# Optimization experiments

Hardware: AMD Instinct MI355X
Metric: run time of the kernel (lower is better)

The kernel has to match this reference:

```python
import jax, jax.numpy as jnp
import numpy as np

N = 50000
E = 1600000
IN = 128
HID = 128
OUT = 64
NL = 200000
NEG_SLOPE = 0.2


def _glorot(key, shape):
    fan_in, fan_out = shape[0], shape[-1]
    s = jnp.sqrt(6.0 / (fan_in + fan_out))
    return jax.random.uniform(key, shape, jnp.float32, -s, s)


def setup_inputs() -> dict:
    key = jax.random.key(0)
    ks = jax.random.split(key, 16)
    x = jax.random.normal(ks[0], (N, IN), jnp.float32)
    edge_index = jax.random.randint(ks[1], (2, E), 0, N, dtype=jnp.int32)
    edge_label_index = jax.random.randint(ks[2], (2, NL), 0, N, dtype=jnp.int32)
    return {
        "x": x,
        "edge_index": edge_index,
        "edge_label_index": edge_label_index,
        "W1": _glorot(ks[3], (IN, HID)),  "a1s": _glorot(ks[4], (HID,)),  "a1d": _glorot(ks[5], (HID,)),  "b1": jnp.zeros((HID,), jnp.float32),
        "W2": _glorot(ks[6], (HID, HID)), "a2s": _glorot(ks[7], (HID,)),  "a2d": _glorot(ks[8], (HID,)),  "b2": jnp.zeros((HID,), jnp.float32),
        "W3": _glorot(ks[9], (HID, HID)), "a3s": _glorot(ks[10], (HID,)), "a3d": _glorot(ks[11], (HID,)), "b3": jnp.zeros((HID,), jnp.float32),
        "W4": _glorot(ks[12], (HID, OUT)), "b4": jnp.zeros((OUT,), jnp.float32),
    }


def _add_self_loops(edge_index, n):
    loop = jnp.arange(n, dtype=edge_index.dtype)
    return jnp.concatenate([edge_index, jnp.stack([loop, loop])], axis=1)


def gat_conv(x, edge_index, W, a_s, a_d, b):
    """PyG GATConv, heads=1, add_self_loops=True: gather, LeakyReLU score,
    segment softmax over destination nodes, scatter-add aggregate."""
    n = x.shape[0]
    ei = _add_self_loops(edge_index, n)
    src, dst = ei[0], ei[1]
    h = x @ W                                    # [N, H]
    e = jax.nn.leaky_relu((h @ a_s)[src] + (h @ a_d)[dst], NEG_SLOPE)  # [E']
    m = jax.ops.segment_max(e, dst, num_segments=n)
    p = jnp.exp(e - m[dst])
    s = jax.ops.segment_sum(p, dst, num_segments=n)
    alpha = p / s[dst]                           # segment softmax
    out = jax.ops.segment_sum(h[src] * alpha[:, None], dst, num_segments=n)
    return out + b


def gcn_conv(x, edge_index, W, b):
    """PyG GCNConv: self-loops + symmetric degree normalization."""
    n = x.shape[0]
    ei = _add_self_loops(edge_index, n)
    src, dst = ei[0], ei[1]
    h = x @ W
    deg = jax.ops.segment_sum(jnp.ones(src.shape, h.dtype), dst, num_segments=n)
    dinv = jax.lax.rsqrt(deg)
    norm = dinv[src] * dinv[dst]                 # [E']
    out = jax.ops.segment_sum(h[src] * norm[:, None], dst, num_segments=n)
    return out + b


def reference(x, edge_index, edge_label_index,
              W1, a1s, a1d, b1, W2, a2s, a2d, b2,
              W3, a3s, a3d, b3, W4, b4):
    h = jax.nn.relu(gat_conv(x, edge_index, W1, a1s, a1d, b1))
    h = jax.nn.relu(gat_conv(h, edge_index, W2, a2s, a2d, b2))
    h = jax.nn.relu(gat_conv(h, edge_index, W3, a3s, a3d, b3))
    z = gcn_conv(h, edge_index, W4, b4)          # [N, OUT]
    # decode: dot product of endpoint embeddings -> link logits [NL]
    return (z[edge_label_index[0]] * z[edge_label_index[1]]).sum(axis=-1)
```

## Files before the change

### kernel.cpp

```cpp
#include <hip/hip_runtime.h>
#include <hip/hip_fp16.h>
#include <math.h>

#define NN   50000
#define NE   1600000
#define DHID 128
#define DOUTC 64
#define NLBL 200000
#define CAP  80
#define NEG  0.2f
#define NBK  196
#define CAPB 8800
#define CHK  4096

typedef unsigned short u16;
typedef _Float16 half8 __attribute__((ext_vector_type(8)));
typedef float floatx4 __attribute__((ext_vector_type(4)));


__global__ __launch_bounds__(256) void k_bin(const int* __restrict__ ei,
                                             int* __restrict__ gcnt,
                                             unsigned* __restrict__ bins) {
    __shared__ int cntL[NBK];
    __shared__ int curL[NBK];
    const int tid = threadIdx.x;
    const int e0 = blockIdx.x * CHK + tid * 16;
    const bool act = (e0 + 15) < NE;

    unsigned pk[16];
    int bb[16];
    if (act) {
#pragma unroll
        for (int g = 0; g < 4; ++g) {
            int4 s4 = *(const int4*)&ei[e0 + g * 4];
            int4 d4 = *(const int4*)&ei[NE + e0 + g * 4];
            int sa[4] = {s4.x, s4.y, s4.z, s4.w};
            int da[4] = {d4.x, d4.y, d4.z, d4.w};
#pragma unroll
            for (int k = 0; k < 4; ++k) {
                int idx = g * 4 + k;
                bb[idx] = da[k] >> 8;
                pk[idx] = (unsigned)sa[k] | ((unsigned)(da[k] & 255) << 16);
            }
        }
    }
    for (int i = tid; i < NBK; i += 256) cntL[i] = 0;
    __syncthreads();
    if (act) {
#pragma unroll
        for (int k = 0; k < 16; ++k) atomicAdd(&cntL[bb[k]], 1);
    }
    __syncthreads();
    for (int i = tid; i < NBK; i += 256) curL[i] = atomicAdd(&gcnt[i], cntL[i]);
    __syncthreads();
    if (act) {
#pragma unroll
        for (int k = 0; k < 16; ++k) {
            int off = atomicAdd(&curL[bb[k]], 1);
            bins[(size_t)bb[k] * CAPB + off] = pk[k];
        }
    }
}

__global__ __launch_bounds__(256) void k_build(const unsigned* __restrict__ bins,
                                               const int* __restrict__ gcnt,
                                               int* __restrict__ cnt,
                                               u16* __restrict__ csr) {
    __shared__ u16 rows[256 * CAP];
    __shared__ int cur[256];
    const int b = blockIdx.x, tid = threadIdx.x;
    const int d0 = b << 8;
    const int nd = min(256, NN - d0);
    if (tid < nd) { cur[tid] = 1; rows[tid * CAP] = (u16)(d0 + tid); }
    __syncthreads();
    const int n = gcnt[b];
    for (int i = tid; i < n; i += 256) {
        unsigned v = bins[(size_t)b * CAPB + i];
        int s = v & 0xFFFF, dl = v >> 16;
        int pos = atomicAdd(&cur[dl], 1);
        if (pos < CAP) rows[dl * CAP + pos] = (u16)s;
    }
    __syncthreads();
    const unsigned* rw = (const unsigned*)rows;
    unsigned* cw = (unsigned*)(csr + (size_t)d0 * CAP);
    const int tot = nd * (CAP / 2);
    for (int i = tid; i < tot; i += 256) cw[i] = rw[i];
    if (tid < nd) cnt[d0 + tid] = cur[tid];
}


__global__ __launch_bounds__(256) void k_prep_w(const float* __restrict__ W1f,
                                                const float* __restrict__ W2f,
                                                const float* __restrict__ W3f,
                                                const float* __restrict__ W4f,
                                                half8* __restrict__ Wf1,
                                                half8* __restrict__ Wf2,
                                                half8* __restrict__ Wf3,
                                                half8* __restrict__ Wf4,
                                                int* __restrict__ gcnt) {
    if (blockIdx.x == 28) {
        int i = threadIdx.x;
        if (i < NBK) gcnt[i] = 0;
        return;
    }
    int e = blockIdx.x * 256 + threadIdx.x;
    const float* W;
    half8* Wf;
    int nout, le;
    if (e < 2048)      { W = W1f; Wf = Wf1; nout = 128; le = e; }
    else if (e < 4096) { W = W2f; Wf = Wf2; nout = 128; le = e - 2048; }
    else if (e < 6144) { W = W3f; Wf = Wf3; nout = 128; le = e - 4096; }
    else               { W = W4f; Wf = Wf4; nout = 64;  le = e - 6144; }
    int c = le >> 8, rem = le & 255, ks = rem >> 6, lane = rem & 63;
    int n = lane & 15, quad = lane >> 4;
    int col = c * 16 + n, k0 = ks * 32 + quad * 8;
    half8 v;
#pragma unroll
    for (int j = 0; j < 8; ++j) v[j] = (_Float16)W[(size_t)(k0 + j) * nout + col];
    Wf[le] = v;
}


template <int NOUT, bool ATTN, typename TA>
__global__ __launch_bounds__(256) void gemm_mfma(const TA* __restrict__ Ain,
                                                 const half8* __restrict__ Wf,
                                                 __half* __restrict__ C16,
                                                 const float* __restrict__ a_s,
                                                 const float* __restrict__ a_d,
                                                 float* __restrict__ asv,
                                                 float* __restrict__ adv, int M) {
    constexpr int CT = NOUT / 16;
    const int tid = threadIdx.x;
    const int wave = tid >> 6, lane = tid & 63;
    const int n = lane & 15, quad = lane >> 4;
    const int row0 = blockIdx.x * 64 + wave * 16;

    const int row = row0 + n;
    const bool ok = row < M;
    half8 a[4];
    half8 zz = {};
#pragma unroll
    for (int ks = 0; ks < 4; ++ks) {
        if (!ok) { a[ks] = zz; continue; }
        if constexpr (sizeof(TA) == 2) {
            a[ks] = *(const half8*)((const _Float16*)Ain + (size_t)row * 128 + quad * 8 + ks * 32);
        } else {
            const float* Ap = (const float*)Ain + (size_t)row * 128 + quad * 8 + ks * 32;
            float4 f0 = *(const float4*)Ap;
            float4 f1 = *(const float4*)(Ap + 4);
            half8 v;
            v[0] = (_Float16)f0.x; v[1] = (_Float16)f0.y; v[2] = (_Float16)f0.z; v[3] = (_Float16)f0.w;
            v[4] = (_Float16)f1.x; v[5] = (_Float16)f1.y; v[6] = (_Float16)f1.z; v[7] = (_Float16)f1.w;
            a[ks] = v;
        }
    }

    floatx4 acc[CT];
#pragma unroll
    for (int c = 0; c < CT; ++c) acc[c] = (floatx4){0.f, 0.f, 0.f, 0.f};

#pragma unroll
    for (int c = 0; c < CT; ++c) {
#pragma unroll
        for (int ks = 0; ks < 4; ++ks) {
            half8 b = Wf[(c * 4 + ks) * 64 + lane];
            acc[c] = __builtin_amdgcn_mfma_f32_16x16x32_f16(b, a[ks], acc[c], 0, 0, 0);
        }
    }

    if (ok) {
#pragma unroll
        for (int c = 0; c < CT; ++c) {
            __half2 h0 = __floats2half2_rn(acc[c][0], acc[c][1]);
            __half2 h1 = __floats2half2_rn(acc[c][2], acc[c][3]);
            uint2 u;
            __builtin_memcpy(&u.x, &h0, 4);
            __builtin_memcpy(&u.y, &h1, 4);
            *(uint2*)&C16[(size_t)row * NOUT + c * 16 + quad * 4] = u;
        }
    }

    if (ATTN) {
        float ps = 0.f, pd = 0.f;
#pragma unroll
        for (int c = 0; c < CT; ++c) {
#pragma unroll
            for (int reg = 0; reg < 4; ++reg) {
                float w = acc[c][reg];
                ps = fmaf(w, a_s[c * 16 + quad * 4 + reg], ps);
                pd = fmaf(w, a_d[c * 16 + quad * 4 + reg], pd);
            }
        }
        ps += __shfl_xor(ps, 16); ps += __shfl_xor(ps, 32);
        pd += __shfl_xor(pd, 16); pd += __shfl_xor(pd, 32);
        if (quad == 0 && ok) { asv[row] = ps; adv[row] = pd; }
    }
}

__device__ inline void fma_h8(uint4 u, float al, float* acc) {
    float2 f0 = __half22float2(*(__half2*)&u.x);
    float2 f1 = __half22float2(*(__half2*)&u.y);
    float2 f2 = __half22float2(*(__half2*)&u.z);
    float2 f3 = __half22float2(*(__half2*)&u.w);
    acc[0] = fmaf(al, f0.x, acc[0]);
    acc[1] = fmaf(al, f0.y, acc[1]);
    acc[2] = fmaf(al, f1.x, acc[2]);
    acc[3] = fmaf(al, f1.y, acc[3]);
    acc[4] = fmaf(al, f2.x, acc[4]);
    acc[5] = fmaf(al, f2.y, acc[5]);
    acc[6] = fmaf(al, f3.x, acc[6]);
    acc[7] = fmaf(al, f3.y, acc[7]);
}


__global__ __launch_bounds__(256) void k_gat_agg(const __half* __restrict__ h,
                                                 const int* __restrict__ cnt,
                                                 const u16* __restrict__ csr,
                                                 const float* __restrict__ asv,
                                                 const float* __restrict__ adv,
                                                 const float* __restrict__ bias,
                                                 __half* __restrict__ outp) {
    __shared__ float alsL[4][88];
    __shared__ int   srcL[4][88];
    int lane = threadIdx.x & 63, wv = threadIdx.x >> 6;
    int d = blockIdx.x * 4 + wv;
    if (d >= NN) return;
    int deg = cnt[d]; if (deg > CAP) deg = CAP;
    const float advd = adv[d];
    const u16* rowp = csr + (size_t)d * CAP;

    int j0 = lane, j1 = lane + 64;
    int s0 = 0, s1 = 0;
    float e0 = -INFINITY, e1 = -INFINITY;
    if (j0 < deg) {
        s0 = rowp[j0];
        float t = asv[s0] + advd;
        e0 = (t >= 0.f) ? t : NEG * t;
    }
    if (j1 < deg) {
        s1 = rowp[j1];
        float t = asv[s1] + advd;
        e1 = (t >= 0.f) ? t : NEG * t;
    }
    float m = fmaxf(e0, e1);
#pragma unroll
    for (int off = 32; off; off >>= 1) m = fmaxf(m, __shfl_xor(m, off));
    float p0 = (j0 < deg) ? __expf(e0 - m) : 0.f;
    float p1 = (j1 < deg) ? __expf(e1 - m) : 0.f;
    float s = p0 + p1;
#pragma unroll
    for (int off = 32; off; off >>= 1) s += __shfl_xor(s, off);
    float inv = 1.f / s;
    alsL[wv][j0] = p0 * inv;
    srcL[wv][j0] = s0;
    if (j1 < 88) { alsL[wv][j1] = p1 * inv; srcL[wv][j1] = s1; }

    int slot = lane >> 3, r = lane & 7;
    float acc[16];
#pragma unroll
    for (int k = 0; k < 16; ++k) acc[k] = 0.f;

    int degp = (deg + 7) & ~7;
    for (int base = 0; base < degp; base += 8) {
        int idx = base + slot;
        float al = alsL[wv][idx];
        int   sj = srcL[wv][idx];
        const uint4* hp = (const uint4*)&h[(size_t)sj * 128 + r * 16];
        uint4 ua = hp[0];
        uint4 ub = hp[1];
        fma_h8(ua, al, acc);
        fma_h8(ub, al, acc + 8);
    }
#pragma unroll
    for (int k = 0; k < 16; ++k) {
        acc[k] += __shfl_xor(acc[k], 8);
        acc[k] += __shfl_xor(acc[k], 16);
        acc[k] += __shfl_xor(acc[k], 32);
    }
    if (slot == 0) {
        __half2 ho[8];
#pragma unroll
        for (int k = 0; k < 8; ++k) {
            float oa = fmaxf(acc[2 * k]     + bias[r * 16 + 2 * k],     0.f);
            float ob = fmaxf(acc[2 * k + 1] + bias[r * 16 + 2 * k + 1], 0.f);
            ho[k] = __floats2half2_rn(oa, ob);
        }
        uint4 u0, u1;
        __builtin_memcpy(&u0, &ho[0], 16);
        __builtin_memcpy(&u1, &ho[4], 16);
        uint4* op = (uint4*)&outp[(size_t)d * 128 + r * 16];
        op[0] = u0; op[1] = u1;
    }
}


__global__ __launch_bounds__(256) void k_gcn_agg(const __half* __restrict__ h,
                                                 const int* __restrict__ cnt,
                                                 const u16* __restrict__ csr,
                                                 const float* __restrict__ bias,
                                                 __half* __restrict__ z) {
    __shared__ float nmL[4][88];
    __shared__ int   srcL[4][88];
    int lane = threadIdx.x & 63, wv = threadIdx.x >> 6;
    int d = blockIdx.x * 4 + wv;
    if (d >= NN) return;
    int degc = cnt[d];
    int deg = degc > CAP ? CAP : degc;
    float did = rsqrtf((float)degc);
    const u16* rowp = csr + (size_t)d * CAP;

    int j0 = lane, j1 = lane + 64;
    int s0 = 0, s1 = 0;
    float n0 = 0.f, n1 = 0.f;
    if (j0 < deg) { s0 = rowp[j0]; n0 = rsqrtf((float)cnt[s0]) * did; }
    if (j1 < deg) { s1 = rowp[j1]; n1 = rsqrtf((float)cnt[s1]) * did; }
    nmL[wv][j0] = n0;
    srcL[wv][j0] = s0;
    if (j1 < 88) { nmL[wv][j1] = n1; srcL[wv][j1] = s1; }

    int slot = lane >> 3, r = lane & 7;
    float acc[8];
#pragma unroll
    for (int k = 0; k < 8; ++k) acc[k] = 0.f;

    int degp = (deg + 7) & ~7;
    for (int base = 0; base < degp; base += 8) {
        int idx = base + slot;
        float nm = nmL[wv][idx];
        int   sj = srcL[wv][idx];
        uint4 u = *(const uint4*)&h[(size_t)sj * 64 + r * 8];
        fma_h8(u, nm, acc);
    }
#pragma unroll
    for (int k = 0; k < 8; ++k) {
        acc[k] += __shfl_xor(acc[k], 8);
        acc[k] += __shfl_xor(acc[k], 16);
        acc[k] += __shfl_xor(acc[k], 32);
    }
    if (slot == 0) {
        __half2 ho[4];
#pragma unroll
        for (int k = 0; k < 4; ++k) {
            float oa = acc[2 * k]     + bias[r * 8 + 2 * k];
            float ob = acc[2 * k + 1] + bias[r * 8 + 2 * k + 1];
            ho[k] = __floats2half2_rn(oa, ob);
        }
        uint2 u0, u1;
        __builtin_memcpy(&u0, &ho[0], 8);
        __builtin_memcpy(&u1, &ho[2], 8);
        uint2* zp = (uint2*)&z[(size_t)d * 64 + r * 8];
        zp[0] = u0; zp[1] = u1;
    }
}


__global__ __launch_bounds__(256) void k_decode(const __half* __restrict__ z,
                                                const int* __restrict__ eli,
                                                float* __restrict__ outp) {
    int lane = threadIdx.x & 63, wv = threadIdx.x >> 6;
    int g = lane >> 4, r = lane & 15;
    int idx = (blockIdx.x * 4 + wv) * 4 + g;
    if (idx >= NLBL) return;
    int a = eli[idx], b = eli[NLBL + idx];
    uint2 ua = *(const uint2*)&z[(size_t)a * 64 + r * 4];
    uint2 ub = *(const uint2*)&z[(size_t)b * 64 + r * 4];
    float2 a0 = __half22float2(*(__half2*)&ua.x);
    float2 a1 = __half22float2(*(__half2*)&ua.y);
    float2 b0 = __half22float2(*(__half2*)&ub.x);
    float2 b1 = __half22float2(*(__half2*)&ub.y);
    float v = a0.x * b0.x + a0.y * b0.y + a1.x * b1.x + a1.y * b1.y;
#pragma unroll
    for (int off = 8; off; off >>= 1) v += __shfl_xor(v, off);
    if (r == 0) outp[idx] = v;
}


extern "C" void kernel_launch(void* const* d_in, const int* in_sizes, int n_in,
                              void* d_out, int out_size, void* d_ws, size_t ws_size,
                              hipStream_t stream) {
    const float* x   = (const float*)d_in[0];
    const int*   ei  = (const int*)d_in[1];
    const int*   eli = (const int*)d_in[2];
    const float* W1 = (const float*)d_in[3];
    const float* a1s = (const float*)d_in[4];
    const float* a1d = (const float*)d_in[5];
    const float* b1 = (const float*)d_in[6];
    const float* W2 = (const float*)d_in[7];
    const float* a2s = (const float*)d_in[8];
    const float* a2d = (const float*)d_in[9];
    const float* b2 = (const float*)d_in[10];
    const float* W3 = (const float*)d_in[11];
    const float* a3s = (const float*)d_in[12];
    const float* a3d = (const float*)d_in[13];
    const float* b3 = (const float*)d_in[14];
    const float* W4 = (const float*)d_in[15];
    const float* b4 = (const float*)d_in[16];
    float* outp = (float*)d_out;

    char* p = (char*)d_ws;
    auto alloc = [&](size_t bytes) -> char* {
        char* r = p;
        p += (bytes + 255) & ~(size_t)255;
        return r;
    };
    int*    cnt  = (int*)alloc((size_t)NN * 4);
    u16*    csr  = (u16*)alloc((size_t)NN * CAP * 2);
    int*    gcnt = (int*)alloc((size_t)NBK * 4);
    float*  asv  = (float*)alloc((size_t)NN * 4);
    float*  advv = (float*)alloc((size_t)NN * 4);
    __half* G    = (__half*)alloc((size_t)NN * 128 * 2);
    __half* Bu1  = (__half*)alloc((size_t)NN * 128 * 2);
    __half* Bu2  = (__half*)alloc((size_t)NN * 128 * 2);
    __half* zf   = (__half*)alloc((size_t)NN * 64 * 2);
    half8*  Wf1  = (half8*)alloc(2048 * 16);
    half8*  Wf2  = (half8*)alloc(2048 * 16);
    half8*  Wf3  = (half8*)alloc(2048 * 16);
    half8*  Wf4  = (half8*)alloc(1024 * 16);
    unsigned* bins = (unsigned*)alloc((size_t)NBK * CAPB * 4);

    const int gBin  = (NE + CHK - 1) / CHK;
    const int gGemm = (NN + 63) / 64;
    const int gNode = (NN + 3) / 4;
    const int gDec  = (NLBL + 15) / 16;

    k_prep_w<<<29, 256, 0, stream>>>(W1, W2, W3, W4, Wf1, Wf2, Wf3, Wf4, gcnt);
    k_bin<<<gBin, 256, 0, stream>>>(ei, gcnt, bins);
    k_build<<<NBK, 256, 0, stream>>>(bins, gcnt, cnt, csr);

    gemm_mfma<128, true, float><<<gGemm, 256, 0, stream>>>(x, Wf1, G, a1s, a1d, asv, advv, NN);
    k_gat_agg<<<gNode, 256, 0, stream>>>(G, cnt, csr, asv, advv, b1, Bu1);

    gemm_mfma<128, true, __half><<<gGemm, 256, 0, stream>>>(Bu1, Wf2, G, a2s, a2d, asv, advv, NN);
    k_gat_agg<<<gNode, 256, 0, stream>>>(G, cnt, csr, asv, advv, b2, Bu2);

    gemm_mfma<128, true, __half><<<gGemm, 256, 0, stream>>>(Bu2, Wf3, G, a3s, a3d, asv, advv, NN);
    k_gat_agg<<<gNode, 256, 0, stream>>>(G, cnt, csr, asv, advv, b3, Bu1);

    gemm_mfma<64, false, __half><<<gGemm, 256, 0, stream>>>(Bu1, Wf4, G, nullptr, nullptr, nullptr, nullptr, NN);
    k_gcn_agg<<<gNode, 256, 0, stream>>>(G, cnt, csr, b4, zf);

    k_decode<<<gDec, 256, 0, stream>>>(zf, eli, outp);
}
```

Baseline: 398.7 us.

## Split 128-wide feature arrays into two 64-column halves for gather cache locality

Node feature arrays (GEMM outputs and GAT aggregation inputs and outputs) are stored as two separate 64-column half buffers instead of one 128-column row-major buffer. The GAT aggregation now runs two passes over the neighbor list, one per half, each gathering 128-byte rows. The aim is a smaller working set per pass, so the random gathers hit L2/MALL more often. The cost is iterating over the edges twice and issuing half-size loads per edge.

```diff
diff --git a/kernel.cpp b/kernel.cpp
--- a/kernel.cpp
+++ b/kernel.cpp
@@ -122,9 +122,11 @@
 
 
 template <int NOUT, bool ATTN, typename TA>
-__global__ __launch_bounds__(256) void gemm_mfma(const TA* __restrict__ Ain,
+__global__ __launch_bounds__(256) void gemm_mfma(const TA* __restrict__ A0,
+                                                 const TA* __restrict__ A1,
                                                  const half8* __restrict__ Wf,
-                                                 __half* __restrict__ C16,
+                                                 __half* __restrict__ C0,
+                                                 __half* __restrict__ C1,
                                                  const float* __restrict__ a_s,
                                                  const float* __restrict__ a_d,
                                                  float* __restrict__ asv,
@@ -142,10 +144,12 @@
 #pragma unroll
     for (int ks = 0; ks < 4; ++ks) {
         if (!ok) { a[ks] = zz; continue; }
+        int c128 = ks * 32 + quad * 8;
         if constexpr (sizeof(TA) == 2) {
-            a[ks] = *(const half8*)((const _Float16*)Ain + (size_t)row * 128 + quad * 8 + ks * 32);
+            const TA* Ah = (c128 < 64) ? A0 : A1;
+            a[ks] = *(const half8*)((const _Float16*)Ah + (size_t)row * 64 + (c128 & 63));
         } else {
-            const float* Ap = (const float*)Ain + (size_t)row * 128 + quad * 8 + ks * 32;
+            const float* Ap = (const float*)A0 + (size_t)row * 128 + c128;
             float4 f0 = *(const float4*)Ap;
             float4 f1 = *(const float4*)(Ap + 4);
             half8 v;
@@ -171,12 +175,14 @@
     if (ok) {
 #pragma unroll
         for (int c = 0; c < CT; ++c) {
+            __half* Ch = (NOUT == 64 || c < 4) ? C0 : C1;
+            int coff = (NOUT == 64 || c < 4) ? c * 16 : (c - 4) * 16;
             __half2 h0 = __floats2half2_rn(acc[c][0], acc[c][1]);
             __half2 h1 = __floats2half2_rn(acc[c][2], acc[c][3]);
             uint2 u;
             __builtin_memcpy(&u.x, &h0, 4);
             __builtin_memcpy(&u.y, &h1, 4);
-            *(uint2*)&C16[(size_t)row * NOUT + c * 16 + quad * 4] = u;
+            *(uint2*)&Ch[(size_t)row * 64 + coff + quad * 4] = u;
         }
     }
 
@@ -197,29 +203,21 @@
     }
 }
 
-__device__ inline void fma_h8(uint4 u, float al, float* acc) {
-    float2 f0 = __half22float2(*(__half2*)&u.x);
-    float2 f1 = __half22float2(*(__half2*)&u.y);
-    float2 f2 = __half22float2(*(__half2*)&u.z);
-    float2 f3 = __half22float2(*(__half2*)&u.w);
-    acc[0] = fmaf(al, f0.x, acc[0]);
-    acc[1] = fmaf(al, f0.y, acc[1]);
-    acc[2] = fmaf(al, f1.x, acc[2]);
-    acc[3] = fmaf(al, f1.y, acc[3]);
-    acc[4] = fmaf(al, f2.x, acc[4]);
-    acc[5] = fmaf(al, f2.y, acc[5]);
-    acc[6] = fmaf(al, f3.x, acc[6]);
-    acc[7] = fmaf(al, f3.y, acc[7]);
-}
-
-
-__global__ __launch_bounds__(256) void k_gat_agg(const __half* __restrict__ h,
+__device__ inline void fma_h8v(half8 h, float al, float* acc) {
+#pragma unroll
+    for (int k = 0; k < 8; ++k) acc[k] = fmaf(al, (float)h[k], acc[k]);
+}
+
+
+__global__ __launch_bounds__(256) void k_gat_agg(const __half* __restrict__ h0,
+                                                 const __half* __restrict__ h1,
                                                  const int* __restrict__ cnt,
                                                  const u16* __restrict__ csr,
                                                  const float* __restrict__ asv,
                                                  const float* __restrict__ adv,
                                                  const float* __restrict__ bias,
-                                                 __half* __restrict__ outp) {
+                                                 __half* __restrict__ out0,
+                                                 __half* __restrict__ out1) {
     __shared__ float alsL[4][88];
     __shared__ int   srcL[4][88];
     int lane = threadIdx.x & 63, wv = threadIdx.x >> 6;
@@ -256,40 +254,40 @@
     if (j1 < 88) { alsL[wv][j1] = p1 * inv; srcL[wv][j1] = s1; }
 
     int slot = lane >> 3, r = lane & 7;
-    float acc[16];
-#pragma unroll
-    for (int k = 0; k < 16; ++k) acc[k] = 0.f;
-
     int degp = (deg + 7) & ~7;
-    for (int base = 0; base < degp; base += 8) {
-        int idx = base + slot;
-        float al = alsL[wv][idx];
-        int   sj = srcL[wv][idx];
-        const uint4* hp = (const uint4*)&h[(size_t)sj * 128 + r * 16];
-        uint4 ua = hp[0];
-        uint4 ub = hp[1];
-        fma_h8(ua, al, acc);
-        fma_h8(ub, al, acc + 8);
-    }
-#pragma unroll
-    for (int k = 0; k < 16; ++k) {
-        acc[k] += __shfl_xor(acc[k], 8);
-        acc[k] += __shfl_xor(acc[k], 16);
-        acc[k] += __shfl_xor(acc[k], 32);
-    }
-    if (slot == 0) {
-        __half2 ho[8];
+#pragma unroll
+    for (int half = 0; half < 2; ++half) {
+        const __half* ht = half ? h1 : h0;
+        __half* ot = half ? out1 : out0;
+        float acc[8];
+#pragma unroll
+        for (int k = 0; k < 8; ++k) acc[k] = 0.f;
+
+        for (int base = 0; base < degp; base += 8) {
+            int idx = base + slot;
+            float al = alsL[wv][idx];
+            int   sj = srcL[wv][idx];
+            half8 hv = *(const half8*)&ht[(size_t)sj * 64 + r * 8];
+            fma_h8v(hv, al, acc);
+        }
 #pragma unroll
         for (int k = 0; k < 8; ++k) {
-            float oa = fmaxf(acc[2 * k]     + bias[r * 16 + 2 * k],     0.f);
-            float ob = fmaxf(acc[2 * k + 1] + bias[r * 16 + 2 * k + 1], 0.f);
-            ho[k] = __floats2half2_rn(oa, ob);
-        }
-        uint4 u0, u1;
-        __builtin_memcpy(&u0, &ho[0], 16);
-        __builtin_memcpy(&u1, &ho[4], 16);
-        uint4* op = (uint4*)&outp[(size_t)d * 128 + r * 16];
-        op[0] = u0; op[1] = u1;
+            acc[k] += __shfl_xor(acc[k], 8);
+            acc[k] += __shfl_xor(acc[k], 16);
+            acc[k] += __shfl_xor(acc[k], 32);
+        }
+        if (slot == 0) {
+            __half2 ho[4];
+#pragma unroll
+            for (int k = 0; k < 4; ++k) {
+                float oa = fmaxf(acc[2 * k]     + bias[half * 64 + r * 8 + 2 * k],     0.f);
+                float ob = fmaxf(acc[2 * k + 1] + bias[half * 64 + r * 8 + 2 * k + 1], 0.f);
+                ho[k] = __floats2half2_rn(oa, ob);
+            }
+            uint4 u;
+            __builtin_memcpy(&u, &ho[0], 16);
+            *(uint4*)&ot[(size_t)d * 64 + r * 8] = u;
+        }
     }
 }
 
@@ -328,8 +326,8 @@
         int idx = base + slot;
         float nm = nmL[wv][idx];
         int   sj = srcL[wv][idx];
-        uint4 u = *(const uint4*)&h[(size_t)sj * 64 + r * 8];
-        fma_h8(u, nm, acc);
+        half8 hv = *(const half8*)&h[(size_t)sj * 64 + r * 8];
+        fma_h8v(hv, nm, acc);
     }
 #pragma unroll
     for (int k = 0; k < 8; ++k) {
@@ -345,11 +343,9 @@
             float ob = acc[2 * k + 1] + bias[r * 8 + 2 * k + 1];
             ho[k] = __floats2half2_rn(oa, ob);
         }
-        uint2 u0, u1;
-        __builtin_memcpy(&u0, &ho[0], 8);
-        __builtin_memcpy(&u1, &ho[2], 8);
-        uint2* zp = (uint2*)&z[(size_t)d * 64 + r * 8];
-        zp[0] = u0; zp[1] = u1;
+        uint4 u;
+        __builtin_memcpy(&u, &ho[0], 16);
+        *(uint4*)&z[(size_t)d * 64 + r * 8] = u;
     }
 }
 
@@ -408,9 +404,12 @@
     int*    gcnt = (int*)alloc((size_t)NBK * 4);
     float*  asv  = (float*)alloc((size_t)NN * 4);
     float*  advv = (float*)alloc((size_t)NN * 4);
-    __half* G    = (__half*)alloc((size_t)NN * 128 * 2);
-    __half* Bu1  = (__half*)alloc((size_t)NN * 128 * 2);
-    __half* Bu2  = (__half*)alloc((size_t)NN * 128 * 2);
+    __half* G0   = (__half*)alloc((size_t)NN * 64 * 2);
+    __half* G1   = (__half*)alloc((size_t)NN * 64 * 2);
+    __half* B1a  = (__half*)alloc((size_t)NN * 64 * 2);
+    __half* B1b  = (__half*)alloc((size_t)NN * 64 * 2);
+    __half* B2a  = (__half*)alloc((size_t)NN * 64 * 2);
+    __half* B2b  = (__half*)alloc((size_t)NN * 64 * 2);
     __half* zf   = (__half*)alloc((size_t)NN * 64 * 2);
     half8*  Wf1  = (half8*)alloc(2048 * 16);
     half8*  Wf2  = (half8*)alloc(2048 * 16);
@@ -427,17 +426,17 @@
     k_bin<<<gBin, 256, 0, stream>>>(ei, gcnt, bins);
     k_build<<<NBK, 256, 0, stream>>>(bins, gcnt, cnt, csr);
 
-    gemm_mfma<128, true, float><<<gGemm, 256, 0, stream>>>(x, Wf1, G, a1s, a1d, asv, advv, NN);
-    k_gat_agg<<<gNode, 256, 0, stream>>>(G, cnt, csr, asv, advv, b1, Bu1);
-
-    gemm_mfma<128, true, __half><<<gGemm, 256, 0, stream>>>(Bu1, Wf2, G, a2s, a2d, asv, advv, NN);
-    k_gat_agg<<<gNode, 256, 0, stream>>>(G, cnt, csr, asv, advv, b2, Bu2);
-
-    gemm_mfma<128, true, __half><<<gGemm, 256, 0, stream>>>(Bu2, Wf3, G, a3s, a3d, asv, advv, NN);
-    k_gat_agg<<<gNode, 256, 0, stream>>>(G, cnt, csr, asv, advv, b3, Bu1);
-
-    gemm_mfma<64, false, __half><<<gGemm, 256, 0, stream>>>(Bu1, Wf4, G, nullptr, nullptr, nullptr, nullptr, NN);
-    k_gcn_agg<<<gNode, 256, 0, stream>>>(G, cnt, csr, b4, zf);
+    gemm_mfma<128, true, float><<<gGemm, 256, 0, stream>>>(x, x, Wf1, G0, G1, a1s, a1d, asv, advv, NN);
+    k_gat_agg<<<gNode, 256, 0, stream>>>(G0, G1, cnt, csr, asv, advv, b1, B1a, B1b);
+
+    gemm_mfma<128, true, __half><<<gGemm, 256, 0, stream>>>(B1a, B1b, Wf2, G0, G1, a2s, a2d, asv, advv, NN);
+    k_gat_agg<<<gNode, 256, 0, stream>>>(G0, G1, cnt, csr, asv, advv, b2, B2a, B2b);
+
+    gemm_mfma<128, true, __half><<<gGemm, 256, 0, stream>>>(B2a, B2b, Wf3, G0, G1, a3s, a3d, asv, advv, NN);
+    k_gat_agg<<<gNode, 256, 0, stream>>>(G0, G1, cnt, csr, asv, advv, b3, B1a, B1b);
+
+    gemm_mfma<64, false, __half><<<gGemm, 256, 0, stream>>>(B1a, B1b, Wf4, G0, G0, nullptr, nullptr, nullptr, nullptr, NN);
+    k_gcn_agg<<<gNode, 256, 0, stream>>>(G0, cnt, csr, b4, zf);
 
     k_decode<<<gDec, 256, 0, stream>>>(zf, eli, outp);
 }
```

Result: faster. 388.1 us (-2.7%).
